# Kernel tuning notes

Hardware: AMD Instinct MI355X
Metric: run time of the kernel (lower is better)

The kernel has to match this reference:

```python
import jax, jax.numpy as jnp
import numpy as np
from jax import lax

ALPHA = 0.42
POOL = 7  # avg_pool2d kernel size (count_include_pad=True -> divide by 49 always)

# fixed 3x3 kernels stacked as [out=3, in=1, 3, 3]: sobel_x, sobel_y, laplacian
_SOBEL_X = np.array([[1, 0, -1], [2, 0, -2], [1, 0, -1]], dtype=np.float32)
_SOBEL_Y = np.array([[1, 2, 1], [0, 0, 0], [-1, -2, -1]], dtype=np.float32)
_LAP = np.array([[0, 1, 0], [1, -4, 1], [0, 1, 0]], dtype=np.float32)
_KERNELS = jnp.asarray(np.stack([_SOBEL_X, _SOBEL_Y, _LAP])[:, None])  # [3,1,3,3]


def setup_inputs() -> dict:
    key = jax.random.key(0)
    k1, k2 = jax.random.split(key)
    logits = jax.random.normal(k1, (16, 3, 1024, 1024), dtype=jnp.float32)
    learnable_weights = jax.random.uniform(k2, (3,), dtype=jnp.float32) * 0.1
    return {"logits": logits, "learnable_weights": learnable_weights}


def _avg_pool_same(x):
    # x: [N, H, W]; torch avg_pool2d(kernel=7, stride=1, padding=3, count_include_pad=True)
    s = lax.reduce_window(x, 0.0, lax.add, (1, POOL, POOL), (1, 1, 1), "SAME")
    return s / (POOL * POOL)


def reference(logits, learnable_weights):
    B, S, H, W = logits.shape
    probs = jax.nn.sigmoid(logits)
    m = probs.reshape(B * S, 1, H, W)  # fold slices into batch -> one grouped conv
    # single conv producing gx, gy, laplacian channels
    conv = lax.conv_general_dilated(
        m, _KERNELS, window_strides=(1, 1), padding="SAME",
        dimension_numbers=("NCHW", "OIHW", "NCHW"))  # [B*S, 3, H, W]
    gx, gy, lp = conv[:, 0], conv[:, 1], conv[:, 2]
    edge = jnp.sqrt(gx * gx + gy * gy) + 0.5 * jnp.abs(lp)  # [B*S, H, W]
    m0 = m[:, 0]
    local_mean = _avg_pool_same(m0)
    local_var = _avg_pool_same((m0 - local_mean) ** 2)
    score = ALPHA * edge.sum((1, 2)) + (1.0 - ALPHA) * local_var.sum((1, 2))
    edge_scores = score.reshape(B, S)
    w_edge = edge_scores / (edge_scores.sum(1, keepdims=True) + 1e-6)
    w_learn = jax.nn.softmax(learnable_weights)  # [S]
    weights = (w_edge + w_learn[None, :]) * 0.5  # [B, S]
    fused = jnp.einsum("bshw,bs->bhw", logits, weights)
    return fused
```

## Files before the change

### kernel.cpp

```cpp
#include <hip/hip_runtime.h>
#include <math.h>

#define ALPHA 0.42f
#define H 1024
#define W 1024
#define NB 16
#define NCH 48
#define BH 64

typedef float nfloat4 __attribute__((ext_vector_type(4)));

__device__ __forceinline__ float sigf(float x) {
    return __builtin_amdgcn_rcpf(1.0f + __expf(-x));
}

__device__ __forceinline__ void block_sync_lds() {
    asm volatile("s_waitcnt lgkmcnt(0)" ::: "memory");
    __builtin_amdgcn_s_barrier();
    asm volatile("" ::: "memory");
}

__global__ __launch_bounds__(256, 3)
void score_kernel(const float* __restrict__ logits, float* __restrict__ scores) {
    __shared__ __align__(16) float lrow[2][1032];
    __shared__ float red[4];
    const int tid  = threadIdx.x;
    const int lane = tid & 63;
    const int wvi  = tid >> 6;
    const int ch   = blockIdx.y;
    const int band = blockIdx.x * BH;
    const int c4   = wvi * 256 + lane * 4;
    const float* img   = logits + (size_t)ch * (H * W);
    const float* gbase = img + c4;

    if (tid < 8) {
        int idx = (tid & 3) + ((tid & 4) ? 1028 : 0);
        lrow[0][idx] = 0.f;
        lrow[1][idx] = 0.f;
    }

    const float cvar  = (1.0f - ALPHA) * (1.0f / 49.0f);
    const float wfxc0 = cvar * (float)(7 - max(0, 3 - (c4 + 0)) - max(0, (c4 + 0) - (W - 4)));
    const float wfxc1 = cvar * (float)(7 - max(0, 3 - (c4 + 1)) - max(0, (c4 + 1) - (W - 4)));
    const float wfxc2 = cvar * (float)(7 - max(0, 3 - (c4 + 2)) - max(0, (c4 + 2) - (W - 4)));
    const float wfxc3 = cvar * (float)(7 - max(0, 3 - (c4 + 3)) - max(0, (c4 + 3) - (W - 4)));

    float4 vb[2];
    float srm[8], sr0[8], sr1[8], sr2[8], sr3[8], srp[8];
    float rsA[8], rsB[8], rsC[8], rsD[8];
    float vs0 = 0.f, vs1 = 0.f, vs2 = 0.f, vs3 = 0.f, acc = 0.f;
    #pragma unroll
    for (int k = 0; k < 8; ++k) { rsA[k] = rsB[k] = rsC[k] = rsD[k] = 0.f; }

    auto LOADROW = [&](int g, int slot) {
        int gc = min(max(g, 0), H - 1);
        vb[slot] = *(const float4*)(gbase + ((size_t)gc << 10));
    };

    auto STEP = [&](int n, int s8, int s2, bool doLoad, bool doEmit) {
        const int g = band - 3 + n;
        float4 raw = vb[s2];
        float q0 = 0.f, q1 = 0.f, q2 = 0.f, q3 = 0.f;
        if (g >= 0 && g < H) {
            q0 = sigf(raw.x); q1 = sigf(raw.y); q2 = sigf(raw.z); q3 = sigf(raw.w);
        }
        *(float4*)&lrow[s2][c4 + 4] = make_float4(q0, q1, q2, q3);
        if (doLoad) LOADROW(g + 2, s2);
        block_sync_lds();
        float4 hl = *(const float4*)&lrow[s2][c4];
        float4 hr = *(const float4*)&lrow[s2][c4 + 8];
        float l1 = hl.y, l2 = hl.z, l3 = hl.w;
        float r0 = hr.x, r1 = hr.y, r2 = hr.z;
        float a = ((l1 + l2) + (l3 + q0)) + ((q1 + q2) + q3);
        float b = a - l1 + r0;
        float c = b - l2 + r1;
        float d = c - l3 + r2;
        const int old = (s8 + 1) & 7;
        vs0 += a - rsA[old]; vs1 += b - rsB[old]; vs2 += c - rsC[old]; vs3 += d - rsD[old];
        rsA[s8] = a; rsB[s8] = b; rsC[s8] = c; rsD[s8] = d;
        srm[s8] = l3; sr0[s8] = q0; sr1[s8] = q1; sr2[s8] = q2; sr3[s8] = q3; srp[s8] = r0;
        if (doEmit) {
            const int Y = g - 3;
            float fy = (float)(7 - max(0, 3 - Y) - max(0, Y - (H - 4)));
            float wf0 = fy * wfxc0, wf1 = fy * wfxc1, wf2 = fy * wfxc2, wf3 = fy * wfxc3;
            const int sA = (s8 + 4) & 7, sB = (s8 + 5) & 7, sC = (s8 + 6) & 7;
            float A0 = srm[sA], A1 = sr0[sA], A2 = sr1[sA], A3 = sr2[sA], A4 = sr3[sA], A5 = srp[sA];
            float B0 = srm[sB], B1 = sr0[sB], B2 = sr1[sB], B3 = sr2[sB], B4 = sr3[sB], B5 = srp[sB];
            float C0 = srm[sC], C1 = sr0[sC], C2 = sr1[sC], C3 = sr2[sC], C4 = sr3[sC], C5 = srp[sC];
            float t0 = A0 + C0, t1 = A1 + C1, t2 = A2 + C2, t3 = A3 + C3, t4 = A4 + C4, t5 = A5 + C5;
            float u0 = A0 - C0, u1 = A1 - C1, u2 = A2 - C2, u3 = A3 - C3, u4 = A4 - C4, u5 = A5 - C5;
            auto PIXF = [&](float tp, float tp1, float tp2, float Bp, float Bp1, float Bp2,
                            float up, float up1, float up2, float vsv, float wf) {
                float sgx = (tp - tp2) + 2.f * (Bp - Bp2);
                float sgy = (up + up2) + 2.f * up1;
                float lp  = (Bp + Bp2) + tp1 - 4.f * Bp1;
                float edge = __builtin_amdgcn_sqrtf(sgx * sgx + sgy * sgy) + 0.5f * fabsf(lp);
                float dd = Bp1 - vsv * (1.f / 49.f);
                acc += ALPHA * edge + wf * (dd * dd);
            };
            PIXF(t0, t1, t2, B0, B1, B2, u0, u1, u2, vs0, wf0);
            PIXF(t1, t2, t3, B1, B2, B3, u1, u2, u3, vs1, wf1);
            PIXF(t2, t3, t4, B2, B3, B4, u2, u3, u4, vs2, wf2);
            PIXF(t3, t4, t5, B3, B4, B5, u3, u4, u5, vs3, wf3);
        }
    };

    LOADROW(band - 3, 0);
    LOADROW(band - 2, 1);
    STEP(0, 0, 0, true, false);
    STEP(1, 1, 1, true, false);
    STEP(2, 2, 0, true, false);
    STEP(3, 3, 1, true, false);
    STEP(4, 4, 0, true, false);
    STEP(5, 5, 1, true, false);
    STEP(6, 6, 0, true, true);
    STEP(7, 7, 1, true, true);
    #pragma unroll 1
    for (int nn = 8; nn < BH; nn += 8) {
        #pragma unroll
        for (int k = 0; k < 8; ++k)
            STEP(nn + k, k, k & 1, true, true);
    }
    STEP(BH + 0, 0, 0, true,  true);
    STEP(BH + 1, 1, 1, true,  true);
    STEP(BH + 2, 2, 0, true,  true);
    STEP(BH + 3, 3, 1, true,  true);
    STEP(BH + 4, 4, 0, false, true);
    STEP(BH + 5, 5, 1, false, true);

    #pragma unroll
    for (int off = 32; off > 0; off >>= 1) acc += __shfl_down(acc, off);
    if (lane == 0) red[wvi] = acc;
    __syncthreads();
    if (tid == 0) atomicAdd(&scores[ch], red[0] + red[1] + red[2] + red[3]);
}

__global__ __launch_bounds__(256)
void fuse_kernel(const float* __restrict__ logits,
                 const float* __restrict__ scores,
                 const float* __restrict__ lw,
                 float* __restrict__ out) {
    const size_t HW4 = (size_t)(H * W) / 4;

    float l0 = lw[0], l1 = lw[1], l2 = lw[2];
    float mx = fmaxf(l0, fmaxf(l1, l2));
    float e0 = __expf(l0 - mx), e1 = __expf(l1 - mx), e2 = __expf(l2 - mx);
    float inv = __builtin_amdgcn_rcpf(e0 + e1 + e2);
    float wl0 = e0 * inv, wl1 = e1 * inv, wl2 = e2 * inv;

    const int b = blockIdx.x >> 8;
    float s0 = scores[b * 3 + 0], s1 = scores[b * 3 + 1], s2 = scores[b * 3 + 2];
    float itot = __builtin_amdgcn_rcpf(s0 + s1 + s2 + 1e-6f);
    float w0 = 0.5f * (s0 * itot + wl0);
    float w1 = 0.5f * (s1 * itot + wl1);
    float w2 = 0.5f * (s2 * itot + wl2);

    size_t i0 = (size_t)blockIdx.x * 1024 + threadIdx.x;
    size_t r  = i0 & (HW4 - 1);
    const nfloat4* pb = (const nfloat4*)logits + (size_t)b * 3 * HW4 + r;
    nfloat4* po = (nfloat4*)out + i0;
    #pragma unroll
    for (int k = 0; k < 4; ++k) {
        nfloat4 x0 = pb[k * 256];
        nfloat4 x1 = pb[k * 256 + HW4];
        nfloat4 x2 = pb[k * 256 + 2 * HW4];
        nfloat4 o = x0 * w0 + x1 * w1 + x2 * w2;
        __builtin_nontemporal_store(o, po + k * 256);
    }
}

extern "C" void kernel_launch(void* const* d_in, const int* in_sizes, int n_in,
                              void* d_out, int out_size, void* d_ws, size_t ws_size,
                              hipStream_t stream) {
    const float* logits = (const float*)d_in[0];
    const float* lw     = (const float*)d_in[1];
    float* out    = (float*)d_out;
    float* scores = (float*)d_ws;

    (void)hipMemsetAsync(d_ws, 0, NCH * sizeof(float), stream);

    dim3 g1(H / BH, NCH);
    score_kernel<<<g1, 256, 0, stream>>>(logits, scores);

    fuse_kernel<<<4096, 256, 0, stream>>>(logits, scores, lw, out);
}
```

Baseline: 333.9 us.

## Merge score and fuse kernels into one cooperative launch with grid sync

Combines the score and weighted-fusion kernels into a single cooperative kernel of 768 blocks that separates the phases with a grid-wide barrier, falling back to two launches if the cooperative launch fails. The fuse phase becomes a grid-stride loop with per-batch weights computed once into shared memory. The row prefetch buffer is widened from two to four slots so global loads are issued further ahead. This aims to remove the second launch gap and let logits stay warm in cache between phases, at the cost of grid-sync overhead and extra register pressure.

Result: slower. 527.1 us (+57.9%).

```diff
diff --git a/kernel.cpp b/kernel.cpp
--- a/kernel.cpp
+++ b/kernel.cpp
@@ -1,10 +1,10 @@
 #include <hip/hip_runtime.h>
+#include <hip/hip_cooperative_groups.h>
 #include <math.h>
 
 #define ALPHA 0.42f
 #define H 1024
 #define W 1024
-#define NB 16
 #define NCH 48
 #define BH 64
 
@@ -20,18 +20,16 @@
     asm volatile("" ::: "memory");
 }
 
-__global__ __launch_bounds__(256, 3)
-void score_kernel(const float* __restrict__ logits, float* __restrict__ scores) {
+__device__ __forceinline__ void score_phase(const float* __restrict__ logits,
+                                            float* __restrict__ scores,
+                                            int bandIdx, int ch, int tid) {
     __shared__ __align__(16) float lrow[2][1032];
     __shared__ float red[4];
-    const int tid  = threadIdx.x;
     const int lane = tid & 63;
     const int wvi  = tid >> 6;
-    const int ch   = blockIdx.y;
-    const int band = blockIdx.x * BH;
+    const int band = bandIdx * BH;
     const int c4   = wvi * 256 + lane * 4;
-    const float* img   = logits + (size_t)ch * (H * W);
-    const float* gbase = img + c4;
+    const float* gbase = logits + (size_t)ch * (H * W) + c4;
 
     if (tid < 8) {
         int idx = (tid & 3) + ((tid & 4) ? 1028 : 0);
@@ -45,7 +43,7 @@
     const float wfxc2 = cvar * (float)(7 - max(0, 3 - (c4 + 2)) - max(0, (c4 + 2) - (W - 4)));
     const float wfxc3 = cvar * (float)(7 - max(0, 3 - (c4 + 3)) - max(0, (c4 + 3) - (W - 4)));
 
-    float4 vb[2];
+    float4 vb[4];
     float srm[8], sr0[8], sr1[8], sr2[8], sr3[8], srp[8];
     float rsA[8], rsB[8], rsC[8], rsD[8];
     float vs0 = 0.f, vs1 = 0.f, vs2 = 0.f, vs3 = 0.f, acc = 0.f;
@@ -57,15 +55,15 @@
         vb[slot] = *(const float4*)(gbase + ((size_t)gc << 10));
     };
 
-    auto STEP = [&](int n, int s8, int s2, bool doLoad, bool doEmit) {
+    auto STEP = [&](int n, int s8, int s4, int s2, bool doLoad, bool doEmit) {
         const int g = band - 3 + n;
-        float4 raw = vb[s2];
+        float4 raw = vb[s4];
         float q0 = 0.f, q1 = 0.f, q2 = 0.f, q3 = 0.f;
         if (g >= 0 && g < H) {
             q0 = sigf(raw.x); q1 = sigf(raw.y); q2 = sigf(raw.z); q3 = sigf(raw.w);
         }
         *(float4*)&lrow[s2][c4 + 4] = make_float4(q0, q1, q2, q3);
-        if (doLoad) LOADROW(g + 2, s2);
+        if (doLoad) LOADROW(g + 4, s4);
         block_sync_lds();
         float4 hl = *(const float4*)&lrow[s2][c4];
         float4 hr = *(const float4*)&lrow[s2][c4 + 8];
@@ -107,26 +105,28 @@
 
     LOADROW(band - 3, 0);
     LOADROW(band - 2, 1);
-    STEP(0, 0, 0, true, false);
-    STEP(1, 1, 1, true, false);
-    STEP(2, 2, 0, true, false);
-    STEP(3, 3, 1, true, false);
-    STEP(4, 4, 0, true, false);
-    STEP(5, 5, 1, true, false);
-    STEP(6, 6, 0, true, true);
-    STEP(7, 7, 1, true, true);
+    LOADROW(band - 1, 2);
+    LOADROW(band + 0, 3);
+    STEP(0, 0, 0, 0, true, false);
+    STEP(1, 1, 1, 1, true, false);
+    STEP(2, 2, 2, 0, true, false);
+    STEP(3, 3, 3, 1, true, false);
+    STEP(4, 4, 0, 0, true, false);
+    STEP(5, 5, 1, 1, true, false);
+    STEP(6, 6, 2, 0, true, true);
+    STEP(7, 7, 3, 1, true, true);
     #pragma unroll 1
     for (int nn = 8; nn < BH; nn += 8) {
         #pragma unroll
         for (int k = 0; k < 8; ++k)
-            STEP(nn + k, k, k & 1, true, true);
-    }
-    STEP(BH + 0, 0, 0, true,  true);
-    STEP(BH + 1, 1, 1, true,  true);
-    STEP(BH + 2, 2, 0, true,  true);
-    STEP(BH + 3, 3, 1, true,  true);
-    STEP(BH + 4, 4, 0, false, true);
-    STEP(BH + 5, 5, 1, false, true);
+            STEP(nn + k, k, k & 3, k & 1, true, true);
+    }
+    STEP(64, 0, 0, 0, true,  true);
+    STEP(65, 1, 1, 1, true,  true);
+    STEP(66, 2, 2, 0, false, true);
+    STEP(67, 3, 3, 1, false, true);
+    STEP(68, 4, 0, 0, false, true);
+    STEP(69, 5, 1, 1, false, true);
 
     #pragma unroll
     for (int off = 32; off > 0; off >>= 1) acc += __shfl_down(acc, off);
@@ -135,38 +135,66 @@
     if (tid == 0) atomicAdd(&scores[ch], red[0] + red[1] + red[2] + red[3]);
 }
 
+__device__ __forceinline__ void fuse_phase(const float* __restrict__ logits,
+                                           const float* __restrict__ scores,
+                                           const float* __restrict__ lw,
+                                           float* __restrict__ out,
+                                           int bid, int tid) {
+    __shared__ float wds[48];
+    if (tid < 16) {
+        float l0 = lw[0], l1 = lw[1], l2 = lw[2];
+        float mx = fmaxf(l0, fmaxf(l1, l2));
+        float e0 = __expf(l0 - mx), e1 = __expf(l1 - mx), e2 = __expf(l2 - mx);
+        float inv = __builtin_amdgcn_rcpf(e0 + e1 + e2);
+        float s0 = __hip_atomic_load(&scores[tid * 3 + 0], __ATOMIC_RELAXED, __HIP_MEMORY_SCOPE_AGENT);
+        float s1 = __hip_atomic_load(&scores[tid * 3 + 1], __ATOMIC_RELAXED, __HIP_MEMORY_SCOPE_AGENT);
+        float s2 = __hip_atomic_load(&scores[tid * 3 + 2], __ATOMIC_RELAXED, __HIP_MEMORY_SCOPE_AGENT);
+        float itot = __builtin_amdgcn_rcpf(s0 + s1 + s2 + 1e-6f);
+        wds[tid * 3 + 0] = 0.5f * (s0 * itot + e0 * inv);
+        wds[tid * 3 + 1] = 0.5f * (s1 * itot + e1 * inv);
+        wds[tid * 3 + 2] = 0.5f * (s2 * itot + e2 * inv);
+    }
+    __syncthreads();
+
+    const size_t NTH = 768 * 256;
+    const size_t TOT = (size_t)16 * 262144;
+    size_t base = (size_t)bid * 256 + tid;
+
+    auto BODY = [&](size_t i) {
+        size_t b = i >> 18;
+        size_t r = i & 262143;
+        float w0 = wds[b * 3 + 0], w1 = wds[b * 3 + 1], w2 = wds[b * 3 + 2];
+        const nfloat4* pb = (const nfloat4*)logits + b * 3 * 262144 + r;
+        nfloat4 x0 = pb[0];
+        nfloat4 x1 = pb[262144];
+        nfloat4 x2 = pb[524288];
+        __builtin_nontemporal_store(x0 * w0 + x1 * w1 + x2 * w2, (nfloat4*)out + i);
+    };
+
+    #pragma unroll 3
+    for (int k = 0; k < 21; ++k) BODY(base + (size_t)k * NTH);
+    size_t i = base + 21 * NTH;
+    if (i < TOT) BODY(i);
+}
+
+__global__ __launch_bounds__(256, 3)
+void fused_kernel(const float* __restrict__ logits, float* __restrict__ scores,
+                  const float* __restrict__ lw, float* __restrict__ out) {
+    score_phase(logits, scores, blockIdx.x, blockIdx.y, threadIdx.x);
+    __threadfence();
+    cooperative_groups::this_grid().sync();
+    fuse_phase(logits, scores, lw, out, blockIdx.y * gridDim.x + blockIdx.x, threadIdx.x);
+}
+
+__global__ __launch_bounds__(256, 3)
+void score_kernel(const float* __restrict__ logits, float* __restrict__ scores) {
+    score_phase(logits, scores, blockIdx.x, blockIdx.y, threadIdx.x);
+}
+
 __global__ __launch_bounds__(256)
-void fuse_kernel(const float* __restrict__ logits,
-                 const float* __restrict__ scores,
-                 const float* __restrict__ lw,
-                 float* __restrict__ out) {
-    const size_t HW4 = (size_t)(H * W) / 4;
-
-    float l0 = lw[0], l1 = lw[1], l2 = lw[2];
-    float mx = fmaxf(l0, fmaxf(l1, l2));
-    float e0 = __expf(l0 - mx), e1 = __expf(l1 - mx), e2 = __expf(l2 - mx);
-    float inv = __builtin_amdgcn_rcpf(e0 + e1 + e2);
-    float wl0 = e0 * inv, wl1 = e1 * inv, wl2 = e2 * inv;
-
-    const int b = blockIdx.x >> 8;
-    float s0 = scores[b * 3 + 0], s1 = scores[b * 3 + 1], s2 = scores[b * 3 + 2];
-    float itot = __builtin_amdgcn_rcpf(s0 + s1 + s2 + 1e-6f);
-    float w0 = 0.5f * (s0 * itot + wl0);
-    float w1 = 0.5f * (s1 * itot + wl1);
-    float w2 = 0.5f * (s2 * itot + wl2);
-
-    size_t i0 = (size_t)blockIdx.x * 1024 + threadIdx.x;
-    size_t r  = i0 & (HW4 - 1);
-    const nfloat4* pb = (const nfloat4*)logits + (size_t)b * 3 * HW4 + r;
-    nfloat4* po = (nfloat4*)out + i0;
-    #pragma unroll
-    for (int k = 0; k < 4; ++k) {
-        nfloat4 x0 = pb[k * 256];
-        nfloat4 x1 = pb[k * 256 + HW4];
-        nfloat4 x2 = pb[k * 256 + 2 * HW4];
-        nfloat4 o = x0 * w0 + x1 * w1 + x2 * w2;
-        __builtin_nontemporal_store(o, po + k * 256);
-    }
+void fuse_kernel(const float* __restrict__ logits, const float* __restrict__ scores,
+                 const float* __restrict__ lw, float* __restrict__ out) {
+    fuse_phase(logits, scores, lw, out, blockIdx.x, threadIdx.x);
 }
 
 extern "C" void kernel_launch(void* const* d_in, const int* in_sizes, int n_in,
@@ -179,8 +207,13 @@
 
     (void)hipMemsetAsync(d_ws, 0, NCH * sizeof(float), stream);
 
-    dim3 g1(H / BH, NCH);
-    score_kernel<<<g1, 256, 0, stream>>>(logits, scores);
-
-    fuse_kernel<<<4096, 256, 0, stream>>>(logits, scores, lw, out);
-}
+    void* args[] = {(void*)&logits, (void*)&scores, (void*)&lw, (void*)&out};
+    hipError_t err = hipLaunchCooperativeKernel((const void*)fused_kernel,
+                                                dim3(H / BH, NCH), dim3(256),
+                                                args, 0, stream);
+    if (err != hipSuccess) {
+        (void)hipGetLastError();
+        score_kernel<<<dim3(H / BH, NCH), 256, 0, stream>>>(logits, scores);
+        fuse_kernel<<<768, 256, 0, stream>>>(logits, scores, lw, out);
+    }
+}
```

## Process row pairs per barrier, halve band height, replace atomics with per-band partials

Applied to the files above, without the earlier changes.

The score kernel now handles two rows per LDS barrier using a 4-slot row buffer and prefetches rows four ahead, which halves the number of block barriers. Band height drops from 64 to 32, doubling the block count, and the occupancy hint rises to 4 blocks. Per-band partial scores are written to workspace and summed in the fuse kernel, which removes the memset launch and the atomics. The trade-off is more halo recomputation (6 of every 38 rows), extra register and LDS pressure, and each fuse block redundantly summing 96 partials.

After: 385.5 us. 15.5% more time.

```diff
diff --git a/kernel.cpp b/kernel.cpp
--- a/kernel.cpp
+++ b/kernel.cpp
@@ -4,9 +4,9 @@
 #define ALPHA 0.42f
 #define H 1024
 #define W 1024
-#define NB 16
 #define NCH 48
-#define BH 64
+#define BH 32
+#define NBANDS (H / BH)
 
 typedef float nfloat4 __attribute__((ext_vector_type(4)));
 
@@ -20,9 +20,9 @@
     asm volatile("" ::: "memory");
 }
 
-__global__ __launch_bounds__(256, 3)
-void score_kernel(const float* __restrict__ logits, float* __restrict__ scores) {
-    __shared__ __align__(16) float lrow[2][1032];
+__global__ __launch_bounds__(256, 4)
+void score_kernel(const float* __restrict__ logits, float* __restrict__ scores_ws) {
+    __shared__ __align__(16) float lrow[4][1032];
     __shared__ float red[4];
     const int tid  = threadIdx.x;
     const int lane = tid & 63;
@@ -30,13 +30,12 @@
     const int ch   = blockIdx.y;
     const int band = blockIdx.x * BH;
     const int c4   = wvi * 256 + lane * 4;
-    const float* img   = logits + (size_t)ch * (H * W);
-    const float* gbase = img + c4;
+    const float* gbase = logits + (size_t)ch * (H * W) + c4;
 
-    if (tid < 8) {
+    if (tid < 32) {
+        int s   = tid >> 3;
         int idx = (tid & 3) + ((tid & 4) ? 1028 : 0);
-        lrow[0][idx] = 0.f;
-        lrow[1][idx] = 0.f;
+        lrow[s][idx] = 0.f;
     }
 
     const float cvar  = (1.0f - ALPHA) * (1.0f / 49.0f);
@@ -45,7 +44,7 @@
     const float wfxc2 = cvar * (float)(7 - max(0, 3 - (c4 + 2)) - max(0, (c4 + 2) - (W - 4)));
     const float wfxc3 = cvar * (float)(7 - max(0, 3 - (c4 + 3)) - max(0, (c4 + 3) - (W - 4)));
 
-    float4 vb[2];
+    float4 vb[4];
     float srm[8], sr0[8], sr1[8], sr2[8], sr3[8], srp[8];
     float rsA[8], rsB[8], rsC[8], rsD[8];
     float vs0 = 0.f, vs1 = 0.f, vs2 = 0.f, vs3 = 0.f, acc = 0.f;
@@ -57,18 +56,10 @@
         vb[slot] = *(const float4*)(gbase + ((size_t)gc << 10));
     };
 
-    auto STEP = [&](int n, int s8, int s2, bool doLoad, bool doEmit) {
-        const int g = band - 3 + n;
-        float4 raw = vb[s2];
-        float q0 = 0.f, q1 = 0.f, q2 = 0.f, q3 = 0.f;
-        if (g >= 0 && g < H) {
-            q0 = sigf(raw.x); q1 = sigf(raw.y); q2 = sigf(raw.z); q3 = sigf(raw.w);
-        }
-        *(float4*)&lrow[s2][c4 + 4] = make_float4(q0, q1, q2, q3);
-        if (doLoad) LOADROW(g + 2, s2);
-        block_sync_lds();
-        float4 hl = *(const float4*)&lrow[s2][c4];
-        float4 hr = *(const float4*)&lrow[s2][c4 + 8];
+    auto INGEST = [&](int m, float q0, float q1, float q2, float q3, int sl, bool doEmit) {
+        const int s8 = m & 7;
+        float4 hl = *(const float4*)&lrow[sl][c4];
+        float4 hr = *(const float4*)&lrow[sl][c4 + 8];
         float l1 = hl.y, l2 = hl.z, l3 = hl.w;
         float r0 = hr.x, r1 = hr.y, r2 = hr.z;
         float a = ((l1 + l2) + (l3 + q0)) + ((q1 + q2) + q3);
@@ -80,7 +71,7 @@
         rsA[s8] = a; rsB[s8] = b; rsC[s8] = c; rsD[s8] = d;
         srm[s8] = l3; sr0[s8] = q0; sr1[s8] = q1; sr2[s8] = q2; sr3[s8] = q3; srp[s8] = r0;
         if (doEmit) {
-            const int Y = g - 3;
+            const int Y = band + m - 6;
             float fy = (float)(7 - max(0, 3 - Y) - max(0, Y - (H - 4)));
             float wf0 = fy * wfxc0, wf1 = fy * wfxc1, wf2 = fy * wfxc2, wf3 = fy * wfxc3;
             const int sA = (s8 + 4) & 7, sB = (s8 + 5) & 7, sC = (s8 + 6) & 7;
@@ -105,55 +96,79 @@
         }
     };
 
+    auto PAIR = [&](int n, bool doEmit, bool doLoad) {
+        const int g   = band - 3 + n;
+        const int sl0 = n & 3, sl1 = (n + 1) & 3;
+        float4 raw0 = vb[sl0];
+        float4 raw1 = vb[sl1];
+        if (doLoad) { LOADROW(g + 4, sl0); LOADROW(g + 5, sl1); }
+        float p0 = 0.f, p1 = 0.f, p2 = 0.f, p3 = 0.f;
+        float q0 = 0.f, q1 = 0.f, q2 = 0.f, q3 = 0.f;
+        if (g >= 0 && g < H) {
+            p0 = sigf(raw0.x); p1 = sigf(raw0.y); p2 = sigf(raw0.z); p3 = sigf(raw0.w);
+        }
+        if (g + 1 >= 0 && g + 1 < H) {
+            q0 = sigf(raw1.x); q1 = sigf(raw1.y); q2 = sigf(raw1.z); q3 = sigf(raw1.w);
+        }
+        *(float4*)&lrow[sl0][c4 + 4] = make_float4(p0, p1, p2, p3);
+        *(float4*)&lrow[sl1][c4 + 4] = make_float4(q0, q1, q2, q3);
+        block_sync_lds();
+        INGEST(n,     p0, p1, p2, p3, sl0, doEmit);
+        INGEST(n + 1, q0, q1, q2, q3, sl1, doEmit);
+    };
+
     LOADROW(band - 3, 0);
     LOADROW(band - 2, 1);
-    STEP(0, 0, 0, true, false);
-    STEP(1, 1, 1, true, false);
-    STEP(2, 2, 0, true, false);
-    STEP(3, 3, 1, true, false);
-    STEP(4, 4, 0, true, false);
-    STEP(5, 5, 1, true, false);
-    STEP(6, 6, 0, true, true);
-    STEP(7, 7, 1, true, true);
+    LOADROW(band - 1, 2);
+    LOADROW(band + 0, 3);
+    PAIR(0, false, true);
+    PAIR(2, false, true);
+    PAIR(4, false, true);
+    PAIR(6, true,  true);
     #pragma unroll 1
-    for (int nn = 8; nn < BH; nn += 8) {
-        #pragma unroll
-        for (int k = 0; k < 8; ++k)
-            STEP(nn + k, k, k & 1, true, true);
+    for (int nn = 8; nn <= 24; nn += 8) {
+        PAIR(nn + 0, true, true);
+        PAIR(nn + 2, true, true);
+        PAIR(nn + 4, true, true);
+        PAIR(nn + 6, true, true);
     }
-    STEP(BH + 0, 0, 0, true,  true);
-    STEP(BH + 1, 1, 1, true,  true);
-    STEP(BH + 2, 2, 0, true,  true);
-    STEP(BH + 3, 3, 1, true,  true);
-    STEP(BH + 4, 4, 0, false, true);
-    STEP(BH + 5, 5, 1, false, true);
+    PAIR(32, true, true);
+    PAIR(34, true, false);
+    PAIR(36, true, false);
 
     #pragma unroll
     for (int off = 32; off > 0; off >>= 1) acc += __shfl_down(acc, off);
     if (lane == 0) red[wvi] = acc;
     __syncthreads();
-    if (tid == 0) atomicAdd(&scores[ch], red[0] + red[1] + red[2] + red[3]);
+    if (tid == 0)
+        scores_ws[ch * NBANDS + blockIdx.x] = red[0] + red[1] + red[2] + red[3];
 }
 
 __global__ __launch_bounds__(256)
 void fuse_kernel(const float* __restrict__ logits,
-                 const float* __restrict__ scores,
+                 const float* __restrict__ scores_ws,
                  const float* __restrict__ lw,
                  float* __restrict__ out) {
     const size_t HW4 = (size_t)(H * W) / 4;
+
+    const int b = blockIdx.x >> 8;
+    const float* sp = scores_ws + (size_t)b * 3 * NBANDS;
+    float s0 = 0.f, s1 = 0.f, s2 = 0.f;
+    #pragma unroll
+    for (int i = 0; i < NBANDS; ++i) {
+        s0 += sp[i];
+        s1 += sp[NBANDS + i];
+        s2 += sp[2 * NBANDS + i];
+    }
 
     float l0 = lw[0], l1 = lw[1], l2 = lw[2];
     float mx = fmaxf(l0, fmaxf(l1, l2));
     float e0 = __expf(l0 - mx), e1 = __expf(l1 - mx), e2 = __expf(l2 - mx);
     float inv = __builtin_amdgcn_rcpf(e0 + e1 + e2);
-    float wl0 = e0 * inv, wl1 = e1 * inv, wl2 = e2 * inv;
-
-    const int b = blockIdx.x >> 8;
-    float s0 = scores[b * 3 + 0], s1 = scores[b * 3 + 1], s2 = scores[b * 3 + 2];
     float itot = __builtin_amdgcn_rcpf(s0 + s1 + s2 + 1e-6f);
-    float w0 = 0.5f * (s0 * itot + wl0);
-    float w1 = 0.5f * (s1 * itot + wl1);
-    float w2 = 0.5f * (s2 * itot + wl2);
+    float w0 = 0.5f * (s0 * itot + e0 * inv);
+    float w1 = 0.5f * (s1 * itot + e1 * inv);
+    float w2 = 0.5f * (s2 * itot + e2 * inv);
 
     size_t i0 = (size_t)blockIdx.x * 1024 + threadIdx.x;
     size_t r  = i0 & (HW4 - 1);
@@ -174,13 +189,11 @@
                               hipStream_t stream) {
     const float* logits = (const float*)d_in[0];
     const float* lw     = (const float*)d_in[1];
-    float* out    = (float*)d_out;
-    float* scores = (float*)d_ws;
+    float* out       = (float*)d_out;
+    float* scores_ws = (float*)d_ws;
 
-    (void)hipMemsetAsync(d_ws, 0, NCH * sizeof(float), stream);
+    dim3 g1(NBANDS, NCH);
+    score_kernel<<<g1, 256, 0, stream>>>(logits, scores_ws);
 
-    dim3 g1(H / BH, NCH);
-    score_kernel<<<g1, 256, 0, stream>>>(logits, scores);
-
-    fuse_kernel<<<4096, 256, 0, stream>>>(logits, scores, lw, out);
+    fuse_kernel<<<4096, 256, 0, stream>>>(logits, scores_ws, lw, out);
 }
```
